# Optimization experiments

Hardware: AMD Instinct MI355X
Metric: run time of the kernel (lower is better)

The kernel has to match this reference:

```python
import jax, jax.numpy as jnp
import numpy as np

B, N, K, D, L = 32, 1024, 16, 256, 256


def setup_inputs() -> dict:
    key = jax.random.key(0)
    k1, k2, k3, k4 = jax.random.split(key, 4)
    targets = jax.random.normal(k1, (B, N, D), dtype=jnp.float32)
    neighbors = jax.random.normal(k2, (B, N, K, D), dtype=jnp.float32)
    a = jax.random.uniform(k3, (B, N, K + 1), dtype=jnp.float32)
    # glorot-uniform-ish kernel
    limit = np.sqrt(6.0 / (D + L)).astype(np.float32)
    kernel = jax.random.uniform(k4, (D, L), dtype=jnp.float32, minval=-limit, maxval=limit)
    return {"targets": targets, "neighbors": neighbors, "a": a, "kernel": kernel}


def reference(targets, neighbors, a, kernel):
    # neighborhood: [B, N, K+1, D] = self node prepended to its K neighbors
    neighborhood = jnp.concatenate([targets[..., None, :], neighbors], axis=-2)
    # matmul with kernel then sum over neighborhood axis (fused via einsum)
    y = jnp.einsum("bnkd,dl->bnl", neighborhood, kernel)  # [B, N, L]
    # degree normalization; guard against isolated nodes (degree ~ 0)
    factor = jnp.sum(a, axis=-1, keepdims=True)  # [B, N, 1]
    factor = jnp.where(factor > 0.5, factor, jnp.ones_like(factor))
    y = y / factor
    # dropout is a no-op at inference; use_bias=False
    return jax.nn.relu(y)
```

## Files before the change

kernel.cpp:

```cpp
#include <hip/hip_runtime.h>


typedef float v4f __attribute__((ext_vector_type(4)));

#define BB 32
#define NN 1024
#define KK 16
#define DD 256
#define LL 256
#define ROWS 32
#define DTILE 16
#define NPASS (DD / DTILE)
#define NTHREADS 256

__device__ __forceinline__ float bcast_lane(float x, int lane) {
    return __int_as_float(__builtin_amdgcn_readlane(__float_as_int(x), lane));
}

__global__ __launch_bounds__(NTHREADS, 4)
void gcn_fused(const float* __restrict__ targets,
               const float* __restrict__ neighbors,
               const float* __restrict__ a,
               const float* __restrict__ kern,
               float* __restrict__ out) {
    __shared__ float kt[2][DTILE * LL];
    __shared__ float invf[ROWS];

    const int t        = threadIdx.x;
    const int w        = t >> 6;
    const int lane     = t & 63;
    const int row_base = blockIdx.x * ROWS;

    const v4f* k4 = (const v4f*)kern;

    v4f stage[4];
    #pragma unroll
    for (int i = 0; i < 4; ++i) stage[i] = k4[i * NTHREADS + t];

    if (t < ROWS) {
        const float* ap = a + (size_t)(row_base + t) * (KK + 1);
        float f = 0.0f;
        #pragma unroll
        for (int j = 0; j < KK + 1; ++j) f += ap[j];
        invf[t] = (f > 0.5f) ? (1.0f / f) : 1.0f;
    }

    const v4f* t4 = (const v4f*)targets;
    const v4f* n4 = (const v4f*)neighbors;
    v4f sreg[8];
    #pragma unroll
    for (int r = 0; r < 8; ++r) {
        const int grow = row_base + w * 8 + r;
        v4f accum = t4[(size_t)grow * (DD / 4) + lane];
        #pragma unroll 4
        for (int k = 0; k < KK; ++k) {
            accum += n4[((size_t)grow * KK + k) * (DD / 4) + lane];
        }
        sreg[r] = accum;
    }

    #pragma unroll
    for (int i = 0; i < 4; ++i)
        *(v4f*)&kt[0][(i * NTHREADS + t) * 4] = stage[i];
    __syncthreads();

    v4f acc[8];
    #pragma unroll
    for (int r = 0; r < 8; ++r) acc[r] = v4f{0.0f, 0.0f, 0.0f, 0.0f};

    for (int dt = 0; dt < NPASS; ++dt) {
        const int cur = dt & 1;
        if (dt < NPASS - 1) {
            #pragma unroll
            for (int i = 0; i < 4; ++i)
                stage[i] = k4[(dt + 1) * (DTILE * LL / 4) + i * NTHREADS + t];
        }
        #pragma unroll
        for (int dd = 0; dd < DTILE; ++dd) {
            v4f kv = *(const v4f*)&kt[cur][dd * LL + 4 * lane];
            const int chunk = dt * (DTILE / 4) + (dd >> 2);
            #pragma unroll
            for (int r = 0; r < 8; ++r) {
                const float sv = bcast_lane(sreg[r][dd & 3], chunk);
                acc[r] += sv * kv;
            }
        }
        if (dt < NPASS - 1) {
            *(v4f*)&kt[cur ^ 1][(0 * NTHREADS + t) * 4] = stage[0];
            *(v4f*)&kt[cur ^ 1][(1 * NTHREADS + t) * 4] = stage[1];
            *(v4f*)&kt[cur ^ 1][(2 * NTHREADS + t) * 4] = stage[2];
            *(v4f*)&kt[cur ^ 1][(3 * NTHREADS + t) * 4] = stage[3];
            __syncthreads();
        }
    }

    #pragma unroll
    for (int r = 0; r < 8; ++r) {
        const int rl    = w * 8 + r;
        const float inv = invf[rl];
        v4f v = acc[r] * inv;
        v.x = fmaxf(v.x, 0.0f);
        v.y = fmaxf(v.y, 0.0f);
        v.z = fmaxf(v.z, 0.0f);
        v.w = fmaxf(v.w, 0.0f);
        __builtin_nontemporal_store(v, (v4f*)&out[(size_t)(row_base + rl) * LL + 4 * lane]);
    }
}

extern "C" void kernel_launch(void* const* d_in, const int* in_sizes, int n_in,
                              void* d_out, int out_size, void* d_ws, size_t ws_size,
                              hipStream_t stream) {
    const float* targets   = (const float*)d_in[0];
    const float* neighbors = (const float*)d_in[1];
    const float* a         = (const float*)d_in[2];
    const float* kern      = (const float*)d_in[3];
    float* out = (float*)d_out;
    const int blocks = (BB * NN) / ROWS;
    gcn_fused<<<dim3(blocks), dim3(NTHREADS), 0, stream>>>(targets, neighbors, a, kern, out);
}
```

Before: 756.6 us.

## Software-pipeline neighbor aggregation with the kernel matmul, two rows at a time

Each wave now processes its 8 rows in four groups of two. While one pair is multiplied against the weight tiles staged in shared memory, the neighbor rows for the next pair are loaded and summed a few at a time. The goal is to hide global-load latency behind the matmul, where before all aggregation ran up front, and to cut the registers holding the aggregated rows. Neighbor and target reads now use nontemporal loads. The cost is that the full weight matrix is streamed through shared memory four times per block, which means more L2 reads and more barriers.

```diff
diff --git a/kernel.cpp b/kernel.cpp
--- a/kernel.cpp
+++ b/kernel.cpp
@@ -10,8 +10,9 @@
 #define LL 256
 #define ROWS 32
 #define DTILE 16
-#define NPASS (DD / DTILE)
+#define NTILES (DD / DTILE)
 #define NTHREADS 256
+#define NG 4
 
 __device__ __forceinline__ float bcast_lane(float x, int lane) {
     return __int_as_float(__builtin_amdgcn_readlane(__float_as_int(x), lane));
@@ -30,8 +31,11 @@
     const int w        = t >> 6;
     const int lane     = t & 63;
     const int row_base = blockIdx.x * ROWS;
+    const int wrow     = row_base + w * 8;
 
     const v4f* k4 = (const v4f*)kern;
+    const v4f* t4 = (const v4f*)targets;
+    const v4f* n4 = (const v4f*)neighbors;
 
     v4f stage[4];
     #pragma unroll
@@ -45,18 +49,19 @@
         invf[t] = (f > 0.5f) ? (1.0f / f) : 1.0f;
     }
 
-    const v4f* t4 = (const v4f*)targets;
-    const v4f* n4 = (const v4f*)neighbors;
-    v4f sreg[8];
-    #pragma unroll
-    for (int r = 0; r < 8; ++r) {
-        const int grow = row_base + w * 8 + r;
-        v4f accum = t4[(size_t)grow * (DD / 4) + lane];
+    v4f sA0, sA1;
+    {
+        const size_t g0 = (size_t)wrow;
+        const size_t g1 = (size_t)wrow + 1;
+        v4f a0 = __builtin_nontemporal_load(&t4[g0 * (DD / 4) + lane]);
+        v4f a1 = __builtin_nontemporal_load(&t4[g1 * (DD / 4) + lane]);
         #pragma unroll 4
         for (int k = 0; k < KK; ++k) {
-            accum += n4[((size_t)grow * KK + k) * (DD / 4) + lane];
+            a0 += __builtin_nontemporal_load(&n4[(g0 * KK + k) * (DD / 4) + lane]);
+            a1 += __builtin_nontemporal_load(&n4[(g1 * KK + k) * (DD / 4) + lane]);
         }
-        sreg[r] = accum;
+        sA0 = a0;
+        sA1 = a1;
     }
 
     #pragma unroll
@@ -68,29 +73,59 @@
     #pragma unroll
     for (int r = 0; r < 8; ++r) acc[r] = v4f{0.0f, 0.0f, 0.0f, 0.0f};
 
-    for (int dt = 0; dt < NPASS; ++dt) {
-        const int cur = dt & 1;
-        if (dt < NPASS - 1) {
+    v4f sB0, sB1, p0, p1;
+
+    #pragma unroll
+    for (int g = 0; g < NG; ++g) {
+        for (int dt = 0; dt < NTILES; ++dt) {
+            const int  cur       = dt & 1;
+            const bool last_pass = (g == NG - 1) && (dt == NTILES - 1);
+
+            if (!last_pass) {
+                const int nxt = (dt + 1) & (NTILES - 1);
+                #pragma unroll
+                for (int i = 0; i < 4; ++i)
+                    stage[i] = k4[nxt * (DTILE * LL / 4) + i * NTHREADS + t];
+            }
+
+            if (g < NG - 1) {
+                if (dt == 0) {
+                    const size_t nrow = (size_t)wrow + 2 * g + 2;
+                    sB0 = __builtin_nontemporal_load(&t4[nrow * (DD / 4) + lane]);
+                    sB1 = __builtin_nontemporal_load(&t4[(nrow + 1) * (DD / 4) + lane]);
+                } else if (dt <= 8) {
+                    sB0 += p0; sB0 += p1;
+                } else {
+                    sB1 += p0; sB1 += p1;
+                }
+                const size_t nrow = (size_t)wrow + 2 * g + 2 + (dt >= 8 ? 1 : 0);
+                const int    k0   = (2 * dt) & 15;
+                p0 = __builtin_nontemporal_load(&n4[(nrow * KK + k0) * (DD / 4) + lane]);
+                p1 = __builtin_nontemporal_load(&n4[(nrow * KK + k0 + 1) * (DD / 4) + lane]);
+            }
+
             #pragma unroll
-            for (int i = 0; i < 4; ++i)
-                stage[i] = k4[(dt + 1) * (DTILE * LL / 4) + i * NTHREADS + t];
-        }
-        #pragma unroll
-        for (int dd = 0; dd < DTILE; ++dd) {
-            v4f kv = *(const v4f*)&kt[cur][dd * LL + 4 * lane];
-            const int chunk = dt * (DTILE / 4) + (dd >> 2);
-            #pragma unroll
-            for (int r = 0; r < 8; ++r) {
-                const float sv = bcast_lane(sreg[r][dd & 3], chunk);
-                acc[r] += sv * kv;
+            for (int dd = 0; dd < DTILE; ++dd) {
+                v4f kv = *(const v4f*)&kt[cur][dd * LL + 4 * lane];
+                const int chunk = dt * (DTILE / 4) + (dd >> 2);
+                const float sv0 = bcast_lane(sA0[dd & 3], chunk);
+                const float sv1 = bcast_lane(sA1[dd & 3], chunk);
+                acc[2 * g]     += sv0 * kv;
+                acc[2 * g + 1] += sv1 * kv;
+            }
+
+            if (!last_pass) {
+                *(v4f*)&kt[cur ^ 1][(0 * NTHREADS + t) * 4] = stage[0];
+                *(v4f*)&kt[cur ^ 1][(1 * NTHREADS + t) * 4] = stage[1];
+                *(v4f*)&kt[cur ^ 1][(2 * NTHREADS + t) * 4] = stage[2];
+                *(v4f*)&kt[cur ^ 1][(3 * NTHREADS + t) * 4] = stage[3];
+                __syncthreads();
             }
         }
-        if (dt < NPASS - 1) {
-            *(v4f*)&kt[cur ^ 1][(0 * NTHREADS + t) * 4] = stage[0];
-            *(v4f*)&kt[cur ^ 1][(1 * NTHREADS + t) * 4] = stage[1];
-            *(v4f*)&kt[cur ^ 1][(2 * NTHREADS + t) * 4] = stage[2];
-            *(v4f*)&kt[cur ^ 1][(3 * NTHREADS + t) * 4] = stage[3];
-            __syncthreads();
+        if (g < NG - 1) {
+            sB1 += p0; sB1 += p1;
+            sA0 = sB0;
+            sA1 = sB1;
         }
     }
 
```

After: 720.9 us. 1.05x faster.
